# Performance work log

Hardware: AMD Instinct MI355X
Metric: run time of the kernel (lower is better)

## Reference

```python
import jax, jax.numpy as jnp
import numpy as np

D = 1024
H = 16
HD = D // H
LN_EPS = 1e-5
RMS_EPS = 1e-6


def layernorm(x, g, b):
    mu = jnp.mean(x, axis=-1, keepdims=True)
    var = jnp.mean(jnp.square(x - mu), axis=-1, keepdims=True)
    return (x - mu) * jax.lax.rsqrt(var + LN_EPS) * g + b


def rmsnorm(x, w):
    ms = jnp.mean(jnp.square(x), axis=-1, keepdims=True)
    return x * jax.lax.rsqrt(ms + RMS_EPS) * w


def setup_inputs() -> dict:
    key = jax.random.key(0)
    ks = jax.random.split(key, 8)
    s = 0.02
    ones = jnp.ones((D,), jnp.float32)
    zeros = jnp.zeros((D,), jnp.float32)
    return {
        "query_tokens": jax.random.normal(ks[0], (4, 512, D), jnp.float32),
        "point_features": jax.random.normal(ks[1], (4, 4096, D), jnp.float32),
        "ln_q_g": ones, "ln_q_b": zeros,
        "ln_kv_g": ones, "ln_kv_b": zeros,
        "Wq": jax.random.normal(ks[2], (D, D), jnp.float32) * s, "bq": zeros,
        "Wk": jax.random.normal(ks[3], (D, D), jnp.float32) * s, "bk": zeros,
        "Wv": jax.random.normal(ks[4], (D, D), jnp.float32) * s, "bv": zeros,
        "rms_q_w": ones, "rms_k_w": ones,
        "Wo": jax.random.normal(ks[5], (D, D), jnp.float32) * s, "bo": zeros,
        "ln_mlp_g": ones, "ln_mlp_b": zeros,
        "W1": jax.random.normal(ks[6], (D, 4 * D), jnp.float32) * s,
        "b1": jnp.zeros((4 * D,), jnp.float32),
        "W2": jax.random.normal(ks[7], (4 * D, D), jnp.float32) * s,
        "b2": zeros,
    }


def reference(query_tokens, point_features, ln_q_g, ln_q_b, ln_kv_g, ln_kv_b,
              Wq, bq, Wk, bk, Wv, bv, rms_q_w, rms_k_w, Wo, bo,
              ln_mlp_g, ln_mlp_b, W1, b1, W2, b2):
    B, K, _ = query_tokens.shape
    N = point_features.shape[1]
    q_in = layernorm(query_tokens, ln_q_g, ln_q_b)
    kv_in = layernorm(point_features, ln_kv_g, ln_kv_b)
    q = rmsnorm(q_in @ Wq + bq, rms_q_w)          # [B,K,D]
    k = rmsnorm(kv_in @ Wk + bk, rms_k_w)         # [B,N,D]
    v = kv_in @ Wv + bv                            # [B,N,D]
    q = q.reshape(B, K, H, HD)
    k = k.reshape(B, N, H, HD)
    v = v.reshape(B, N, H, HD)
    scores = jnp.einsum('bkhd,bnhd->bhkn', q, k) / jnp.sqrt(jnp.float32(HD))
    attn = jax.nn.softmax(scores, axis=-1)
    ctx = jnp.einsum('bhkn,bnhd->bkhd', attn, v).reshape(B, K, D)
    out = ctx @ Wo + bo + query_tokens
    h = layernorm(out, ln_mlp_g, ln_mlp_b)
    mlp = jax.nn.gelu(h @ W1 + b1, approximate=False) @ W2 + b2
    return out + mlp
```

## Files before the change

kernel.cpp:

```cpp
#include <hip/hip_runtime.h>
#include <math.h>

#define DD   1024
#define NHD  16
#define HDIM 64
#define BB   4
#define QN   512
#define KVN  4096
#define FF   4096

typedef __attribute__((ext_vector_type(8))) short bf16x8;
typedef __attribute__((ext_vector_type(4))) float f32x4;

__device__ __forceinline__ float b2f(ushort u){
  union { unsigned u32; float f; } x; x.u32 = ((unsigned)u)<<16; return x.f;
}
__device__ __forceinline__ ushort f2b(float f){
  unsigned u = __float_as_uint(f);
  unsigned r = (u + 0x7FFFu + ((u>>16)&1u)) >> 16;
  return (ushort)r;
}
__device__ __forceinline__ float ldx(const void* p, size_t i, int isbf){
  return isbf ? b2f(((const ushort*)p)[i]) : ((const float*)p)[i];
}
__device__ __forceinline__ int detect_bf(const void* gref){
  return ((const unsigned*)gref)[0] == 0x3F803F80u;
}

#if defined(__has_builtin)
#if __has_builtin(__builtin_amdgcn_global_load_lds)
#define HAS_GLL 1
#endif
#endif
#ifndef HAS_GLL
#define HAS_GLL 0
#endif
__device__ __forceinline__ void stage16(const ushort* g, ushort* lds_base, int lane){
#if HAS_GLL
  __builtin_amdgcn_global_load_lds(g, lds_base, 16, 0, 0);
#else
  *(uint4*)(lds_base + lane*8) = *(const uint4*)g;
#endif
}

__global__ __launch_bounds__(256)
void trans_all(const void* __restrict__ Wq, const void* __restrict__ Wk,
               const void* __restrict__ Wv, const void* __restrict__ Wo,
               const void* __restrict__ W1, const void* __restrict__ W2,
               ushort* __restrict__ WqT, ushort* __restrict__ WkvT,
               ushort* __restrict__ WoT,
               ushort* __restrict__ W1T, ushort* __restrict__ W2T,
               const void* __restrict__ gref)
{
  const int isbf = detect_bf(gref);
  int bid = blockIdx.x;
  const void* src; ushort* dst; int R, C, tid;
  if (bid < 1024){
    int s = bid >> 8; tid = bid & 255; R = 1024; C = 1024;
    src = (s==0) ? Wq : (s==1) ? Wk : (s==2) ? Wv : Wo;
    dst = (s==0) ? WqT : (s==1) ? WkvT : (s==2) ? (WkvT + (size_t)1024*1024) : WoT;
  } else if (bid < 2048){ tid = bid - 1024; src = W1; dst = W1T; R = 1024; C = 4096; }
  else                  { tid = bid - 2048; src = W2; dst = W2T; R = 4096; C = 1024; }
  int ntx = C >> 6;
  int tx = tid % ntx, ty = tid / ntx;
  int r0 = ty*64, c0 = tx*64;

  __shared__ __align__(16) ushort tile[64][72];
  int t = threadIdx.x;
  if (isbf){
    #pragma unroll
    for (int i=0;i<2;i++){
      int idx = t + i*256;
      int r = idx>>3, ch = idx&7;
      #pragma unroll
      for (int j=0;j<8;j++)
        tile[r][ch*8+j] = ((const ushort*)src)[(size_t)(r0+r)*C + c0 + ch*8 + j];
    }
  } else {
    #pragma unroll
    for (int i=0;i<2;i++){
      int idx = t + i*256;
      int r = idx>>3, ch = idx&7;
      const float* s4 = (const float*)src + (size_t)(r0+r)*C + c0 + ch*8;
      float4 f0 = *(const float4*)s4;
      float4 f1 = *(const float4*)(s4+4);
      tile[r][ch*8+0]=f2b(f0.x); tile[r][ch*8+1]=f2b(f0.y);
      tile[r][ch*8+2]=f2b(f0.z); tile[r][ch*8+3]=f2b(f0.w);
      tile[r][ch*8+4]=f2b(f1.x); tile[r][ch*8+5]=f2b(f1.y);
      tile[r][ch*8+6]=f2b(f1.z); tile[r][ch*8+7]=f2b(f1.w);
    }
  }
  __syncthreads();
  #pragma unroll
  for (int i=0;i<2;i++){
    int idx = t + i*256;
    int c = idx>>3, ch = idx&7;
    __align__(16) ushort tmp[8];
    #pragma unroll
    for (int j=0;j<8;j++) tmp[j] = tile[ch*8+j][c];
    *(uint4*)(dst + (size_t)(c0+c)*R + r0 + ch*8) = *(uint4*)tmp;
  }
}

__global__ __launch_bounds__(256)
void ln_all(const void* __restrict__ qtok, const void* __restrict__ pfeat,
            const void* __restrict__ gq, const void* __restrict__ bq,
            const void* __restrict__ gkv, const void* __restrict__ bkv,
            ushort* __restrict__ q_ln, ushort* __restrict__ kv_ln,
            const void* __restrict__ gref)
{
  const int isbf = detect_bf(gref);
  int row = blockIdx.x, t = threadIdx.x;
  const void* src; const void* g; const void* bb; ushort* dst; int r;
  if (row < BB*QN){ src = qtok;  g = gq;  bb = bq;  dst = q_ln;  r = row; }
  else            { src = pfeat; g = gkv; bb = bkv; dst = kv_ln; r = row - BB*QN; }
  int c0 = t*4;
  float v[4];
  if (isbf){
    #pragma unroll
    for (int i=0;i<4;i++) v[i] = b2f(((const ushort*)src)[(size_t)r*DD + c0 + i]);
  } else {
    float4 f = *(const float4*)((const float*)src + (size_t)r*DD + c0);
    v[0]=f.x; v[1]=f.y; v[2]=f.z; v[3]=f.w;
  }
  float s1=0.f, s2=0.f;
  #pragma unroll
  for (int i=0;i<4;i++){ s1 += v[i]; s2 += v[i]*v[i]; }
  #pragma unroll
  for (int off=32; off; off>>=1){ s1 += __shfl_xor(s1,off,64); s2 += __shfl_xor(s2,off,64); }
  __shared__ float r1[4], r2[4];
  int wave = t>>6;
  if ((t&63)==0){ r1[wave]=s1; r2[wave]=s2; }
  __syncthreads();
  s1 = r1[0]+r1[1]+r1[2]+r1[3];
  s2 = r2[0]+r2[1]+r2[2]+r2[3];
  float mu  = s1 * (1.0f/DD);
  float var = s2 * (1.0f/DD) - mu*mu;
  float rs  = rsqrtf(var + 1e-5f);
  union { ushort u[4]; uint2 w; } pk;
  #pragma unroll
  for (int i=0;i<4;i++)
    pk.u[i] = f2b((v[i]-mu)*rs*ldx(g,c0+i,isbf) + ldx(bb,c0+i,isbf));
  *(uint2*)(dst + (size_t)r*DD + c0) = pk.w;
}

__global__ __launch_bounds__(256)
void ln_f32(const float* __restrict__ x, const void* __restrict__ g,
            const void* __restrict__ bb, ushort* __restrict__ y,
            const void* __restrict__ gref)
{
  const int isbf = detect_bf(gref);
  int row = blockIdx.x, t = threadIdx.x;
  int c0 = t*4;
  float4 f = *(const float4*)(x + (size_t)row*DD + c0);
  float v[4] = {f.x, f.y, f.z, f.w};
  float s1=0.f, s2=0.f;
  #pragma unroll
  for (int i=0;i<4;i++){ s1 += v[i]; s2 += v[i]*v[i]; }
  #pragma unroll
  for (int off=32; off; off>>=1){ s1 += __shfl_xor(s1,off,64); s2 += __shfl_xor(s2,off,64); }
  __shared__ float r1[4], r2[4];
  int wave = t>>6;
  if ((t&63)==0){ r1[wave]=s1; r2[wave]=s2; }
  __syncthreads();
  s1 = r1[0]+r1[1]+r1[2]+r1[3];
  s2 = r2[0]+r2[1]+r2[2]+r2[3];
  float mu  = s1 * (1.0f/DD);
  float var = s2 * (1.0f/DD) - mu*mu;
  float rs  = rsqrtf(var + 1e-5f);
  union { ushort u[4]; uint2 w; } pk;
  #pragma unroll
  for (int i=0;i<4;i++)
    pk.u[i] = f2b((v[i]-mu)*rs*ldx(g,c0+i,isbf) + ldx(bb,c0+i,isbf));
  *(uint2*)(y + (size_t)row*DD + c0) = pk.w;
}

__global__ __launch_bounds__(256)
void rms_all(ushort* __restrict__ qb, const void* __restrict__ wq,
             ushort* __restrict__ kb, const void* __restrict__ wk,
             const void* __restrict__ gref)
{
  const int isbf = detect_bf(gref);
  int row = blockIdx.x, t = threadIdx.x;
  ushort* x; const void* w; int r;
  if (row < BB*QN){ x = qb; w = wq; r = row; }
  else            { x = kb; w = wk; r = row - BB*QN; }
  int c0 = t*4;
  union { ushort u[4]; uint2 w; } in;
  in.w = *(const uint2*)(x + (size_t)r*DD + c0);
  float v[4];
  #pragma unroll
  for (int i=0;i<4;i++) v[i] = b2f(in.u[i]);
  float s2 = 0.f;
  #pragma unroll
  for (int i=0;i<4;i++) s2 += v[i]*v[i];
  #pragma unroll
  for (int off=32; off; off>>=1) s2 += __shfl_xor(s2,off,64);
  __shared__ float r2[4];
  int wave = t>>6;
  if ((t&63)==0) r2[wave]=s2;
  __syncthreads();
  s2 = r2[0]+r2[1]+r2[2]+r2[3];
  float rs = rsqrtf(s2*(1.0f/DD) + 1e-6f);
  union { ushort u[4]; uint2 w; } pk;
  #pragma unroll
  for (int i=0;i<4;i++) pk.u[i] = f2b(v[i]*rs*ldx(w,c0+i,isbf));
  *(uint2*)(x + (size_t)r*DD + c0) = pk.w;
}

template<int ACT_GELU, int OUT_MODE, int RES_MODE>
__global__ __launch_bounds__(256)
void gemm_bt(const ushort* __restrict__ A, const ushort* __restrict__ BT,
             const void* __restrict__ bias,
             const void* __restrict__ res_ext, const float* __restrict__ res_f,
             void* __restrict__ Cout, void* __restrict__ Cout2,
             int M, int N, int Kdim,
             const void* __restrict__ gref)
{
  const int isbf = detect_bf(gref);
  __shared__ __align__(16) ushort As[128*64];
  __shared__ __align__(16) ushort Bs[128*64];
  const int bm = blockIdx.y * 128;
  const int bn = blockIdx.x * 128;
  const int t = threadIdx.x;
  const int wave = t>>6, lane = t&63, quad = lane>>4, l16 = lane&15;
  const int wm = (wave&1)*64, wn = (wave>>1)*64;

  const ushort* ga[4]; const ushort* gb[4];
  #pragma unroll
  for (int j=0;j<4;j++){
    int row = (t>>3) + j*32;
    int g = ((t&7) - row) & 7;
    ga[j] = A  + (size_t)(bm+row)*Kdim + g*8;
    gb[j] = BT + (size_t)(bn+row)*Kdim + g*8;
  }

  int offA[2][4], offB[2][4];
  #pragma unroll
  for (int kk=0;kk<2;kk++)
    #pragma unroll
    for (int i=0;i<4;i++){
      int ra = wm + i*16 + l16;
      offA[kk][i] = ra*64 + ((quad + kk*4 + ra)&7)*8;
      int rb = wn + i*16 + l16;
      offB[kk][i] = rb*64 + ((quad + kk*4 + rb)&7)*8;
    }

  f32x4 zero = {0.f,0.f,0.f,0.f};
  f32x4 acc[4][4];
  #pragma unroll
  for (int i=0;i<4;i++)
    #pragma unroll
    for (int j=0;j<4;j++) acc[i][j] = zero;

  const int kiters = Kdim >> 6;
  for (int ki = 0; ki < kiters; ki++) {
    #pragma unroll
    for (int j=0;j<4;j++){
      stage16(ga[j], As + (size_t)(j*256 + wave*64)*8, lane);
      stage16(gb[j], Bs + (size_t)(j*256 + wave*64)*8, lane);
      ga[j] += 64; gb[j] += 64;
    }
    __syncthreads();
    #pragma unroll
    for (int kk=0;kk<2;kk++){
      bf16x8 af[4], bfr[4];
      #pragma unroll
      for (int i=0;i<4;i++){
        af[i]  = *(const bf16x8*)(As + offA[kk][i]);
        bfr[i] = *(const bf16x8*)(Bs + offB[kk][i]);
      }
      #pragma unroll
      for (int mt=0;mt<4;mt++)
        #pragma unroll
        for (int nt=0;nt<4;nt++)
          acc[mt][nt] = __builtin_amdgcn_mfma_f32_16x16x32_bf16(af[mt], bfr[nt], acc[mt][nt], 0,0,0);
    }
    __syncthreads();
  }

  if (OUT_MODE == 3){
    if (bn < 1024){
      float bv[4];
      #pragma unroll
      for (int nt=0;nt<4;nt++) bv[nt] = ldx(bias, bn + wn + nt*16 + l16, isbf);
      ushort* kout = (ushort*)Cout;
      #pragma unroll
      for (int mt=0;mt<4;mt++){
        #pragma unroll
        for (int r=0;r<4;r++){
          int row = bm + wm + mt*16 + quad*4 + r;
          #pragma unroll
          for (int nt=0;nt<4;nt++){
            int col = bn + wn + nt*16 + l16;
            kout[(size_t)row*1024 + col] = f2b(acc[mt][nt][r] + bv[nt]);
          }
        }
      }
    } else {
      float bv[4];
      #pragma unroll
      for (int nt=0;nt<4;nt++) bv[nt] = ldx(res_ext, bn-1024 + wn + nt*16 + l16, isbf);
      ushort* Vt = (ushort*)Cout2;
      #pragma unroll
      for (int mt=0;mt<4;mt++){
        int row0 = bm + wm + mt*16 + quad*4;
        int b = row0 >> 12, tok = row0 & (KVN-1);
        #pragma unroll
        for (int nt=0;nt<4;nt++){
          int cl = bn-1024 + wn + nt*16 + l16;
          union { ushort u[4]; uint2 w; } pk;
          #pragma unroll
          for (int r=0;r<4;r++) pk.u[r] = f2b(acc[mt][nt][r] + bv[nt]);
          size_t o = ((size_t)((b*NHD + (cl>>6))*HDIM + (cl&63)))*KVN + tok;
          *(uint2*)(Vt + o) = pk.w;
        }
      }
    }
    return;
  }

  float bv[4];
  #pragma unroll
  for (int nt=0;nt<4;nt++) bv[nt] = ldx(bias, bn + wn + nt*16 + l16, isbf);
  #pragma unroll
  for (int mt=0;mt<4;mt++){
    #pragma unroll
    for (int r=0;r<4;r++){
      int row = bm + wm + mt*16 + quad*4 + r;
      #pragma unroll
      for (int nt=0;nt<4;nt++){
        int col = bn + wn + nt*16 + l16;
        float v = acc[mt][nt][r] + bv[nt];
        if (ACT_GELU) v = 0.5f*v*(1.0f + erff(v*0.70710678118f));
        size_t oi = (size_t)row*N + col;
        if (RES_MODE==1) v += ldx(res_ext, oi, isbf);
        if (RES_MODE==2) v += res_f[oi];
        if (OUT_MODE==0)      ((ushort*)Cout)[oi] = f2b(v);
        else if (OUT_MODE==1) ((float*)Cout)[oi]  = v;
        else { if (isbf) ((ushort*)Cout)[oi] = f2b(v); else ((float*)Cout)[oi] = v; }
      }
    }
  }
}

__global__ __launch_bounds__(256, 3)
void flash_attn3(const ushort* __restrict__ Q, const ushort* __restrict__ K,
                 const ushort* __restrict__ Vt, float* __restrict__ Op,
                 float* __restrict__ ML)
{
  __shared__ __align__(16) ushort Ks[128*72];
  __shared__ __align__(16) ushort Vs[64*136];
  __shared__ __align__(16) ushort Ps[4][16*136];
  const int bh = blockIdx.x, qt = blockIdx.y, hf = blockIdx.z;
  const int b = bh>>4, h = bh&15;
  const int t = threadIdx.x, wave = t>>6, lane = t&63, quad = lane>>4, l16 = lane&15;
  ushort* Pz = Ps[wave];

  const float QS = 0.125f * 1.4426950408889634f;
  bf16x8 qf[2][2];
  #pragma unroll
  for (int mt=0;mt<2;mt++){
    const ushort* qb = Q + (size_t)(b*QN + qt*128 + wave*32 + mt*16 + l16)*DD + h*HDIM;
    bf16x8 r0 = *(const bf16x8*)(qb + quad*8);
    bf16x8 r1 = *(const bf16x8*)(qb + 32 + quad*8);
    #pragma unroll
    for (int j=0;j<8;j++){
      qf[mt][0][j] = (short)f2b(b2f((ushort)r0[j]) * QS);
      qf[mt][1][j] = (short)f2b(b2f((ushort)r1[j]) * QS);
    }
  }

  f32x4 zero = {0.f,0.f,0.f,0.f};
  f32x4 o[2][4];
  #pragma unroll
  for (int mt=0;mt<2;mt++)
    #pragma unroll
    for (int nt=0;nt<4;nt++) o[mt][nt] = zero;
  float lp[2][4] = {{0.f,0.f,0.f,0.f},{0.f,0.f,0.f,0.f}};

  const ushort* kgb = K  + (size_t)(b*KVN + hf*1024)*DD + h*HDIM;
  const ushort* vtb = Vt + ((size_t)bh*HDIM)*KVN + hf*1024;
  const int kcs = t&7;

  for (int kv0 = 0; kv0 < 1024; kv0 += 128) {
    #pragma unroll
    for (int j=0;j<4;j++){
      int kr = (t>>3) + j*32;
      *(uint4*)(Ks + kr*72 + kcs*8) =
        *(const uint4*)(kgb + (size_t)(kv0+kr)*DD + kcs*8);
    }
    #pragma unroll
    for (int j=0;j<4;j++){
      int p = t + j*256; int vr = p>>4, vc = p&15;
      uint4 d = *(const uint4*)(vtb + (size_t)vr*KVN + kv0 + vc*8);
      ushort* pv = (ushort*)&d;
      ushort* vbp = Vs + vr*136 + (vc&1)*64 + (vc>>1);
      #pragma unroll
      for (int jj=0;jj<8;jj++) vbp[jj*8] = pv[jj];
    }
    __syncthreads();

    f32x4 pb[2][8];
    #pragma unroll
    for (int nt=0;nt<8;nt++){
      const ushort* kb = Ks + (nt*16+l16)*72 + quad*8;
      bf16x8 kf0 = *(const bf16x8*)kb;
      bf16x8 kf1 = *(const bf16x8*)(kb + 32);
      #pragma unroll
      for (int mt=0;mt<2;mt++){
        f32x4 a = __builtin_amdgcn_mfma_f32_16x16x32_bf16(qf[mt][0], kf0, zero, 0,0,0);
        a = __builtin_amdgcn_mfma_f32_16x16x32_bf16(qf[mt][1], kf1, a, 0,0,0);
        #pragma unroll
        for (int r=0;r<4;r++) a[r] = __builtin_amdgcn_exp2f(fminf(a[r], 88.f));
        pb[mt][nt] = a;
      }
    }
    #pragma unroll
    for (int mt=0;mt<2;mt++){
      #pragma unroll
      for (int r=0;r<4;r++){
        float ls = 0.f;
        bf16x8 pk;
        #pragma unroll
        for (int nt=0;nt<8;nt++){
          ls += pb[mt][nt][r];
          pk[nt] = (short)(__float_as_uint(pb[mt][nt][r]) >> 16);
        }
        lp[mt][r] += ls;
        *(bf16x8*)(Pz + (quad*4+r)*136 + l16*8) = pk;
      }
      #pragma unroll
      for (int kc=0;kc<4;kc++){
        bf16x8 pa = *(const bf16x8*)(Pz + l16*136 + kc*32 + quad*8);
        pb[mt][kc] = *(f32x4*)&pa;
      }
    }
    #pragma unroll
    for (int nt=0;nt<4;nt++){
      const ushort* vbr = Vs + (nt*16+l16)*136;
      #pragma unroll
      for (int kc=0;kc<4;kc++){
        bf16x8 vf = *(const bf16x8*)(vbr + kc*32 + quad*8);
        o[0][nt] = __builtin_amdgcn_mfma_f32_16x16x32_bf16(*(bf16x8*)&pb[0][kc], vf, o[0][nt], 0,0,0);
        o[1][nt] = __builtin_amdgcn_mfma_f32_16x16x32_bf16(*(bf16x8*)&pb[1][kc], vf, o[1][nt], 0,0,0);
      }
    }
    __syncthreads();
  }

  const int slot = hf*256 + bh*4 + qt;
  float* Ob = Op + (size_t)slot*128*64;
  #pragma unroll
  for (int mt=0;mt<2;mt++)
    #pragma unroll
    for (int nt=0;nt<4;nt++)
      #pragma unroll
      for (int r=0;r<4;r++)
        Ob[(wave*32 + mt*16 + quad*4 + r)*64 + nt*16 + l16] = o[mt][nt][r];
  #pragma unroll
  for (int mt=0;mt<2;mt++)
    #pragma unroll
    for (int r=0;r<4;r++){
      float v = lp[mt][r];
      #pragma unroll
      for (int off=1; off<16; off<<=1) v += __shfl_xor(v, off, 64);
      if (l16 == 0)
        ML[(size_t)slot*128 + wave*32 + mt*16 + quad*4 + r] = v;
    }
}

__global__ __launch_bounds__(256)
void flash_combine4(const float* __restrict__ Op, const float* __restrict__ ML,
                    ushort* __restrict__ Ctx)
{
  const int bq = blockIdx.x;
  const int bh = bq>>2, qt = bq&3;
  const int b = bh>>4, h = bh&15;
  const int t = threadIdx.x;
  const int row = t>>1, hd0 = (t&1)*32;
  float l = 0.f;
  #pragma unroll
  for (int i=0;i<4;i++) l += ML[(size_t)(i*256 + bq)*128 + row];
  float inv = 1.0f / l;
  float4 a[8];
  #pragma unroll
  for (int c=0;c<8;c++){ a[c].x=0.f; a[c].y=0.f; a[c].z=0.f; a[c].w=0.f; }
  #pragma unroll
  for (int i=0;i<4;i++){
    const float* s = Op + ((size_t)(i*256 + bq)*128 + row)*64 + hd0;
    #pragma unroll
    for (int c=0;c<8;c++){
      float4 v = *(const float4*)(s + c*4);
      a[c].x += v.x; a[c].y += v.y; a[c].z += v.z; a[c].w += v.w;
    }
  }
  ushort* dst = Ctx + (size_t)(b*QN + qt*128 + row)*DD + h*HDIM + hd0;
  #pragma unroll
  for (int c=0;c<8;c++){
    union { ushort u[4]; uint2 w; } pk;
    pk.u[0] = f2b(a[c].x*inv); pk.u[1] = f2b(a[c].y*inv);
    pk.u[2] = f2b(a[c].z*inv); pk.u[3] = f2b(a[c].w*inv);
    *(uint2*)(dst + c*4) = pk.w;
  }
}

extern "C" void kernel_launch(void* const* d_in, const int* in_sizes, int n_in,
                              void* d_out, int out_size, void* d_ws, size_t ws_size,
                              hipStream_t stream)
{
  const void* qtok    = d_in[0];
  const void* pfeat   = d_in[1];
  const void* ln_q_g  = d_in[2];
  const void* ln_q_b  = d_in[3];
  const void* ln_kv_g = d_in[4];
  const void* ln_kv_b = d_in[5];
  const void* Wq      = d_in[6];
  const void* bq      = d_in[7];
  const void* Wk      = d_in[8];
  const void* bk      = d_in[9];
  const void* Wv      = d_in[10];
  const void* bv      = d_in[11];
  const void* rms_q_w = d_in[12];
  const void* rms_k_w = d_in[13];
  const void* Wo      = d_in[14];
  const void* bo      = d_in[15];
  const void* ln_mlp_g= d_in[16];
  const void* ln_mlp_b= d_in[17];
  const void* W1      = d_in[18];
  const void* b1      = d_in[19];
  const void* W2      = d_in[20];
  const void* b2      = d_in[21];
  const void* gref    = ln_q_g;

  char* w = (char*)d_ws;
  auto take = [&](size_t bytes)->char*{ char* p = w; w += (bytes + 255) & ~(size_t)255; return p; };
  ushort* WqT  = (ushort*)take((size_t)DD*DD*2);
  ushort* WkvT = (ushort*)take((size_t)2*DD*DD*2);
  ushort* WoT  = (ushort*)take((size_t)DD*DD*2);
  ushort* W1T  = (ushort*)take((size_t)DD*FF*2);
  ushort* W2T  = (ushort*)take((size_t)FF*DD*2);
  ushort* kv_ln= (ushort*)take((size_t)BB*KVN*DD*2);
  ushort* q_ln = (ushort*)take((size_t)BB*QN*DD*2);
  ushort* kbuf = (ushort*)take((size_t)BB*KVN*DD*2);
  ushort* qbuf = (ushort*)take((size_t)BB*QN*DD*2);
  ushort* Vt   = (ushort*)take((size_t)BB*KVN*DD*2);
  ushort* ctx  = WqT;
  float*  outb = (float*)kbuf;
  ushort* mlp1 = kv_ln;
  ushort* h_ln = q_ln;
  float*  Op   = (float*)kv_ln;
  float*  ML   = (float*)q_ln;

  trans_all<<<3072,256,0,stream>>>(Wq,Wk,Wv,Wo,W1,W2, WqT,WkvT,WoT,W1T,W2T, gref);
  ln_all<<<BB*QN + BB*KVN,256,0,stream>>>(qtok,pfeat, ln_q_g,ln_q_b, ln_kv_g,ln_kv_b,
                                          q_ln, kv_ln, gref);
  gemm_bt<0,0,0><<<dim3(8,16), 256,0,stream>>>(q_ln,  WqT, bq, nullptr,nullptr,
                                               qbuf, nullptr, BB*QN, DD, DD, gref);
  gemm_bt<0,3,0><<<dim3(16,128),256,0,stream>>>(kv_ln, WkvT, bk, bv, nullptr,
                                                kbuf, Vt, BB*KVN, 2*DD, DD, gref);
  rms_all<<<BB*QN + BB*KVN,256,0,stream>>>(qbuf, rms_q_w, kbuf, rms_k_w, gref);
  flash_attn3<<<dim3(64,4,4),256,0,stream>>>(qbuf, kbuf, Vt, Op, ML);
  flash_combine4<<<256,256,0,stream>>>(Op, ML, ctx);
  gemm_bt<0,1,1><<<dim3(8,16),256,0,stream>>>(ctx, WoT, bo, qtok, nullptr,
                                              outb, nullptr, BB*QN, DD, DD, gref);
  ln_f32<<<BB*QN,256,0,stream>>>(outb, ln_mlp_g, ln_mlp_b, h_ln, gref);
  gemm_bt<1,0,0><<<dim3(32,16),256,0,stream>>>(h_ln, W1T, b1, nullptr,nullptr,
                                               mlp1, nullptr, BB*QN, FF, DD, gref);
  gemm_bt<0,2,2><<<dim3(8,16), 256,0,stream>>>(mlp1, W2T, b2, nullptr, outb,
                                               d_out, nullptr, BB*QN, DD, FF, gref);
}
```

Baseline: 577.3 us.

## Replace KV projection GEMM with 256x256-tile pipelined 8-wave kernel

Adds a dedicated 256x256 tile GEMM for the fused K/V projection using 512 threads, double-buffered LDS staged with direct global-to-LDS loads, a swizzled layout, and interleaved load/MFMA phases with priority hints and explicit waitcnts. It targets the largest GEMM (16384x2048x1024) to raise MFMA utilisation and overlap memory with compute compared with the generic tile kernel. The epilogue writes K row-major and V transposed as before. It uses 128 KB of LDS per block and fragile hand-scheduled synchronisation.

```diff
diff --git a/kernel.cpp b/kernel.cpp
--- a/kernel.cpp
+++ b/kernel.cpp
@@ -43,6 +43,12 @@
 #endif
 }
 
+__device__ __forceinline__ void wave_barrier(){
+  asm volatile("" ::: "memory");
+  __builtin_amdgcn_s_barrier();
+  asm volatile("" ::: "memory");
+}
+
 __global__ __launch_bounds__(256)
 void trans_all(const void* __restrict__ Wq, const void* __restrict__ Wk,
                const void* __restrict__ Wv, const void* __restrict__ Wo,
@@ -339,6 +345,172 @@
         if (OUT_MODE==0)      ((ushort*)Cout)[oi] = f2b(v);
         else if (OUT_MODE==1) ((float*)Cout)[oi]  = v;
         else { if (isbf) ((ushort*)Cout)[oi] = f2b(v); else ((float*)Cout)[oi] = v; }
+      }
+    }
+  }
+}
+
+#define G_HB  32768
+#define G_RA0 0
+#define G_RA1 8192
+#define G_RB0 16384
+#define G_RB1 24576
+
+#define G_STAGE(src, R, tile) do{ \
+  ushort* _d = ldsb + (((tile)&1)*G_HB + (R) + wave*1024); \
+  stage16(src[0] + ((tile)<<6), _d,       lane); \
+  stage16(src[1] + ((tile)<<6), _d + 512, lane); \
+}while(0)
+
+#define G_LDA(dst, base) \
+  _Pragma("unroll") for (int kk=0;kk<2;kk++) \
+  _Pragma("unroll") for (int m=0;m<4;m++) \
+    dst[kk][m] = *(const bf16x8*)((base) + offA[kk][m]);
+
+#define G_LDB(dst, base) \
+  _Pragma("unroll") for (int kk=0;kk<2;kk++) \
+  _Pragma("unroll") for (int n=0;n<2;n++) \
+    dst[kk][n] = *(const bf16x8*)((base) + offB[kk][n]);
+
+#define G_MM16(ar, br, MO, NO) \
+  _Pragma("unroll") for (int kk=0;kk<2;kk++) \
+  _Pragma("unroll") for (int m=0;m<4;m++) \
+  _Pragma("unroll") for (int n=0;n<2;n++) \
+    acc[m+(MO)][n+(NO)] = __builtin_amdgcn_mfma_f32_16x16x32_bf16(ar[kk][m], br[kk][n], acc[m+(MO)][n+(NO)], 0,0,0);
+
+#define G_SYNC() do{ wave_barrier(); \
+  asm volatile("s_waitcnt lgkmcnt(0)" ::: "memory"); \
+  __builtin_amdgcn_sched_barrier(0); \
+  __builtin_amdgcn_s_setprio(1); }while(0)
+
+#define G_END() do{ __builtin_amdgcn_s_setprio(0); wave_barrier(); }while(0)
+
+__global__ __launch_bounds__(512, 2)
+void gemm256_kv(const ushort* __restrict__ A, const ushort* __restrict__ BT,
+                const void* __restrict__ biasK, const void* __restrict__ biasV,
+                ushort* __restrict__ Kout, ushort* __restrict__ Vt,
+                int Kdim, const void* __restrict__ gref)
+{
+  const int isbf = detect_bf(gref);
+  __shared__ __align__(16) ushort ldsb[65536];
+  const int bm = blockIdx.y * 256;
+  const int bn = blockIdx.x * 256;
+  const int t = threadIdx.x;
+  const int wave = t>>6, lane = t&63, quad = lane>>4, l16 = lane&15;
+  const int wg = wave>>2, wn = wave&3;
+
+  const ushort *sA0[2], *sA1[2], *sB0[2], *sB1[2];
+  #pragma unroll
+  for (int jj=0;jj<2;jj++){
+    int r = (wave*2 + jj)*8 + (lane>>3);
+    int g = ((lane&7) - r) & 7;
+    int grA0 = r + (r & 64);
+    int gc0  = (r & 31) + ((r >> 5) << 6);
+    sA0[jj] = A  + (size_t)(bm + grA0     )*Kdim + g*8;
+    sA1[jj] = A  + (size_t)(bm + grA0 + 64)*Kdim + g*8;
+    sB0[jj] = BT + (size_t)(bn + gc0      )*Kdim + g*8;
+    sB1[jj] = BT + (size_t)(bn + gc0 + 32 )*Kdim + g*8;
+  }
+
+  int offA[2][4], offB[2][2];
+  #pragma unroll
+  for (int kk=0;kk<2;kk++){
+    int slot = ((kk*4 + quad + l16) & 7) * 8;
+    #pragma unroll
+    for (int m=0;m<4;m++) offA[kk][m] = (wg*64 + m*16 + l16)*64 + slot;
+    #pragma unroll
+    for (int n=0;n<2;n++) offB[kk][n] = (wn*32 + n*16 + l16)*64 + slot;
+  }
+
+  f32x4 zero = {0.f,0.f,0.f,0.f};
+  f32x4 acc[8][4];
+  #pragma unroll
+  for (int i=0;i<8;i++)
+    #pragma unroll
+    for (int j=0;j<4;j++) acc[i][j] = zero;
+
+  G_STAGE(sA0, G_RA0, 0);
+  G_STAGE(sB0, G_RB0, 0);
+  G_STAGE(sB1, G_RB1, 0);
+  G_STAGE(sA1, G_RA1, 0);
+  G_STAGE(sA0, G_RA0, 1);
+  G_STAGE(sB1, G_RB1, 1);
+  G_STAGE(sA1, G_RA1, 1);
+  asm volatile("s_waitcnt vmcnt(6)" ::: "memory");
+  wave_barrier();
+
+  const int niter = Kdim >> 7;
+  const ushort* L0 = ldsb;
+  const ushort* L1 = ldsb + G_HB;
+  bf16x8 a[2][4], b[2][2], b1[2][2];
+
+  for (int i = 0; i < niter; ++i) {
+    const bool st = (i + 1 < niter);
+    G_LDA(a, L0 + G_RA0); G_LDB(b, L0 + G_RB0);
+    G_STAGE(sB0, G_RB0, 2*i+1);
+    G_SYNC(); G_MM16(a, b, 0, 0); G_END();
+    G_LDB(b1, L0 + G_RB1);
+    if (st) G_STAGE(sA0, G_RA0, 2*i+2);
+    G_SYNC(); G_MM16(a, b1, 0, 2); G_END();
+    G_LDA(a, L0 + G_RA1);
+    if (st) G_STAGE(sB1, G_RB1, 2*i+2);
+    G_SYNC(); G_MM16(a, b1, 4, 2); G_END();
+    G_LDB(b, L0 + G_RB0);
+    if (st) G_STAGE(sA1, G_RA1, 2*i+2);
+    G_SYNC(); G_MM16(a, b, 4, 0);
+    __builtin_amdgcn_s_setprio(0);
+    if (st) { asm volatile("s_waitcnt vmcnt(6)" ::: "memory"); }
+    else    { asm volatile("s_waitcnt vmcnt(0)" ::: "memory"); }
+    wave_barrier();
+    G_LDA(a, L1 + G_RA0); G_LDB(b, L1 + G_RB0);
+    if (st) G_STAGE(sB0, G_RB0, 2*i+2);
+    G_SYNC(); G_MM16(a, b, 0, 0); G_END();
+    G_LDB(b1, L1 + G_RB1);
+    if (st) G_STAGE(sA0, G_RA0, 2*i+3);
+    G_SYNC(); G_MM16(a, b1, 0, 2); G_END();
+    G_LDA(a, L1 + G_RA1);
+    if (st) G_STAGE(sB1, G_RB1, 2*i+3);
+    G_SYNC(); G_MM16(a, b1, 4, 2); G_END();
+    G_LDB(b, L1 + G_RB0);
+    if (st) G_STAGE(sA1, G_RA1, 2*i+3);
+    G_SYNC(); G_MM16(a, b, 4, 0);
+    __builtin_amdgcn_s_setprio(0);
+    if (st) { asm volatile("s_waitcnt vmcnt(6)" ::: "memory"); }
+    wave_barrier();
+  }
+
+  if (bn < 1024){
+    float bvv[4];
+    #pragma unroll
+    for (int nt=0;nt<4;nt++) bvv[nt] = ldx(biasK, bn + wn*64 + nt*16 + l16, isbf);
+    #pragma unroll
+    for (int mt=0;mt<8;mt++){
+      #pragma unroll
+      for (int r=0;r<4;r++){
+        int row = bm + wg*128 + mt*16 + quad*4 + r;
+        #pragma unroll
+        for (int nt=0;nt<4;nt++){
+          int col = bn + wn*64 + nt*16 + l16;
+          Kout[(size_t)row*1024 + col] = f2b(acc[mt][nt][r] + bvv[nt]);
+        }
+      }
+    }
+  } else {
+    float bvv[4];
+    #pragma unroll
+    for (int nt=0;nt<4;nt++) bvv[nt] = ldx(biasV, bn - 1024 + wn*64 + nt*16 + l16, isbf);
+    #pragma unroll
+    for (int mt=0;mt<8;mt++){
+      int row0 = bm + wg*128 + mt*16 + quad*4;
+      int bi = row0 >> 12, tok = row0 & (KVN-1);
+      #pragma unroll
+      for (int nt=0;nt<4;nt++){
+        int cl = bn - 1024 + wn*64 + nt*16 + l16;
+        union { ushort u[4]; uint2 w2; } pk;
+        #pragma unroll
+        for (int r=0;r<4;r++) pk.u[r] = f2b(acc[mt][nt][r] + bvv[nt]);
+        size_t o = ((size_t)((bi*NHD + (cl>>6))*HDIM + (cl&63)))*KVN + tok;
+        *(uint2*)(Vt + o) = pk.w2;
       }
     }
   }
@@ -557,8 +729,8 @@
                                           q_ln, kv_ln, gref);
   gemm_bt<0,0,0><<<dim3(8,16), 256,0,stream>>>(q_ln,  WqT, bq, nullptr,nullptr,
                                                qbuf, nullptr, BB*QN, DD, DD, gref);
-  gemm_bt<0,3,0><<<dim3(16,128),256,0,stream>>>(kv_ln, WkvT, bk, bv, nullptr,
-                                                kbuf, Vt, BB*KVN, 2*DD, DD, gref);
+  gemm256_kv<<<dim3(2*DD/256, BB*KVN/256), 512, 0, stream>>>(kv_ln, WkvT, bk, bv,
+                                                             kbuf, Vt, DD, gref);
   rms_all<<<BB*QN + BB*KVN,256,0,stream>>>(qbuf, rms_q_w, kbuf, rms_k_w, gref);
   flash_attn3<<<dim3(64,4,4),256,0,stream>>>(qbuf, kbuf, Vt, Op, ML);
   flash_combine4<<<256,256,0,stream>>>(Op, ML, ctx);
```

Result: no change. 577.1 us (-0.0%).
